# Kernel optimization log

Measured on AMD Instinct MI355X. Metric: run time of the kernel, lower is better.

## Reference

```python
import jax, jax.numpy as jnp
import numpy as np

B, S, D = 4, 2048, 1024


def setup_inputs() -> dict:
    key = jax.random.key(0)
    ks = jax.random.split(key, 9)
    scale = 1.0 / np.sqrt(D)
    v = jax.random.normal(ks[0], (B, S, D), dtype=jnp.float32)
    k = jax.random.normal(ks[1], (B, S, D), dtype=jnp.float32)
    q = jax.random.normal(ks[2], (B, S, D), dtype=jnp.float32)
    # causal boolean mask broadcast over batch: [B, S, S]
    mask = jnp.broadcast_to(jnp.tril(jnp.ones((S, S), dtype=bool)), (B, S, S))
    Wq = jax.random.normal(ks[3], (D, D), dtype=jnp.float32) * scale
    bq = jnp.zeros((D,), dtype=jnp.float32)
    Wk = jax.random.normal(ks[4], (D, D), dtype=jnp.float32) * scale
    bk = jnp.zeros((D,), dtype=jnp.float32)
    Wv = jax.random.normal(ks[5], (D, D), dtype=jnp.float32) * scale
    bv = jnp.zeros((D,), dtype=jnp.float32)
    return {"v": v, "k": k, "q": q, "mask": mask,
            "Wq": Wq, "bq": bq, "Wk": Wk, "bk": bk, "Wv": Wv, "bv": bv}


def reference(v, k, q, mask, Wq, bq, Wk, bk, Wv, bv):
    # Dense projections (flax Dense: x @ W + b)
    qp = jnp.einsum('bsd,de->bse', q, Wq) + bq
    kp = jnp.einsum('bsd,de->bse', k, Wk) + bk
    vp = jnp.einsum('bsd,de->bse', v, Wv) + bv
    inv_sqrt_d = jnp.float32(1.0 / np.sqrt(D))
    scores = jnp.einsum('bqd,bkd->bqk', qp, kp) * inv_sqrt_d  # [B,S,S]
    scores = jnp.where(mask, scores, jnp.float32(-1e10))
    attn = jax.nn.softmax(scores, axis=-1)
    return qp + jnp.einsum('bqk,bkd->bqd', attn, vp)
```

## Files before the change

kernel.cpp:

```cpp
#include <hip/hip_runtime.h>
#include <hip/hip_bf16.h>
#include <stdint.h>
#include <stddef.h>


using bf16 = __hip_bfloat16;
typedef __attribute__((ext_vector_type(8))) short short8;
typedef __attribute__((ext_vector_type(4))) float f32x4;

#define B_ 4
#define S_ 2048
#define D_ 1024
#define NTOK (B_ * S_)
#define NELEM ((size_t)NTOK * D_)

__device__ __forceinline__ float bits_to_f(unsigned short h) {
  union { unsigned int u; float f; } c;
  c.u = ((unsigned int)h) << 16;
  return c.f;
}

__device__ __forceinline__ void gld_lds16(const void* g, void* l) {
  __builtin_amdgcn_global_load_lds(
      (const __attribute__((address_space(1))) unsigned int*)g,
      (__attribute__((address_space(3))) unsigned int*)l, 16, 0, 0);
}

__global__ void detect_kernel(const unsigned short* __restrict__ qraw,
                              int* __restrict__ flag) {
  const int lane = threadIdx.x;
  const float v = fabsf(bits_to_f(qraw[2 * lane]));
  const bool sane = (v < 64.0f) && (v == 0.0f || v > 1e-30f);
  const unsigned long long m = __ballot(sane);
  if (lane == 0) *flag = (__popcll(m) >= 56) ? 1 : 0;
}

__global__ __launch_bounds__(256) void zero_kernel(float* __restrict__ p) {
  p[blockIdx.x * 256 + threadIdx.x] = 0.f;
}

__global__ __launch_bounds__(256) void convert_kernel(
    const void* __restrict__ v, const void* __restrict__ k,
    const void* __restrict__ q, bf16* __restrict__ dst,
    const int* __restrict__ flag) {
  const int z = blockIdx.z;
  const void* src = (z == 0) ? v : (z == 1) ? k : q;
  bf16* d = dst + (size_t)z * NELEM;
  const size_t i = (size_t)blockIdx.x * 256 + threadIdx.x;
  const int mode = *flag;
  if (mode) {
    ((uint4*)d)[i] = ((const uint4*)src)[i];
  } else {
    const float4 a = ((const float4*)src)[2 * i];
    const float4 b = ((const float4*)src)[2 * i + 1];
    __align__(16) bf16 t[8];
    t[0] = __float2bfloat16(a.x); t[1] = __float2bfloat16(a.y);
    t[2] = __float2bfloat16(a.z); t[3] = __float2bfloat16(a.w);
    t[4] = __float2bfloat16(b.x); t[5] = __float2bfloat16(b.y);
    t[6] = __float2bfloat16(b.z); t[7] = __float2bfloat16(b.w);
    ((uint4*)d)[i] = *(const uint4*)t;
  }
}

__global__ __launch_bounds__(256) void transpose_kernel(
    const void* __restrict__ Wq, const void* __restrict__ Wk,
    const void* __restrict__ Wv, bf16* __restrict__ WT,
    const int* __restrict__ flag) {
  __shared__ bf16 t[32][33];
  const int z = blockIdx.z;
  const void* W = (z == 0) ? Wq : (z == 1) ? Wk : Wv;
  bf16* O = WT + (size_t)z * D_ * D_;
  const int bx = blockIdx.x * 32, by = blockIdx.y * 32;
  const int tx = threadIdx.x, ty = threadIdx.y;
  const int mode = *flag;
#pragma unroll
  for (int i = 0; i < 32; i += 8) {
    const size_t idx = (size_t)(by + ty + i) * D_ + bx + tx;
    const float val = mode ? __bfloat162float(((const bf16*)W)[idx])
                           : ((const float*)W)[idx];
    t[ty + i][tx] = __float2bfloat16(val);
  }
  __syncthreads();
#pragma unroll
  for (int i = 0; i < 32; i += 8)
    O[(size_t)(bx + ty + i) * D_ + by + tx] = t[tx][ty + i];
}

__device__ __forceinline__ void gemm128_core(
    const bf16* __restrict__ A, int lda, int m0,
    const bf16* __restrict__ Bt, int ldb, int n0,
    int kEnd, bf16* As, bf16* Bs, f32x4 acc[4][4])
{
  const int tid  = threadIdx.x;
  const int wave = tid >> 6;
  const int lane = tid & 63;
  const int srow = lane >> 2;
  const int scol = (lane & 3) * 8;
  const int wm = (wave & 1) * 64;
  const int wn = (wave >> 1) * 64;
  const int fr = lane & 15;
  const int fk = (lane >> 4) * 8;

  for (int k0 = 0; k0 < kEnd; k0 += 32) {
    __syncthreads();
#pragma unroll
    for (int i = 0; i < 2; ++i) {
      const int r0 = (i * 4 + wave) * 16;
      gld_lds16(A  + (size_t)(m0 + r0 + srow) * lda + k0 + scol, As + r0 * 32);
      gld_lds16(Bt + (size_t)(n0 + r0 + srow) * ldb + k0 + scol, Bs + r0 * 32);
    }
    __syncthreads();
    short8 a[4], b[4];
#pragma unroll
    for (int t = 0; t < 4; ++t) {
      a[t] = *(const short8*)(As + (wm + t * 16 + fr) * 32 + fk);
      b[t] = *(const short8*)(Bs + (wn + t * 16 + fr) * 32 + fk);
    }
#pragma unroll
    for (int mt = 0; mt < 4; ++mt)
#pragma unroll
      for (int nt = 0; nt < 4; ++nt)
        acc[mt][nt] = __builtin_amdgcn_mfma_f32_16x16x32_bf16(
            a[mt], b[nt], acc[mt][nt], 0, 0, 0);
  }
}

__global__ __launch_bounds__(256) void proj_kernel(
    const bf16* __restrict__ xc,
    const bf16* __restrict__ WT,
    const void* __restrict__ bq, const void* __restrict__ bk,
    const void* __restrict__ bv,
    bf16* __restrict__ qp, bf16* __restrict__ kp, bf16* __restrict__ vpt,
    const int* __restrict__ flag)
{
  __shared__ bf16 As[128 * 32];
  __shared__ bf16 Bs[128 * 32];
  const int z = blockIdx.z;
  const bf16* A    = xc + (size_t)(z == 0 ? 2 : (z == 1 ? 1 : 0)) * NELEM;
  const void* bias = (z == 0) ? bq : (z == 1) ? bk : bv;
  const bf16* Bt = WT + (size_t)z * D_ * D_;
  const int m0 = blockIdx.x * 128, n0 = blockIdx.y * 128;
  const int mode = *flag;

  f32x4 acc[4][4] = {};
  gemm128_core(A, D_, m0, Bt, D_, n0, D_, As, Bs, acc);

  const int lane = threadIdx.x & 63, wave = threadIdx.x >> 6;
  const int wm = (wave & 1) * 64, wn = (wave >> 1) * 64;
  const int ccol = lane & 15, crow = (lane >> 4) * 4;
#pragma unroll
  for (int mt = 0; mt < 4; ++mt)
#pragma unroll
    for (int nt = 0; nt < 4; ++nt)
#pragma unroll
      for (int i = 0; i < 4; ++i) {
        const int m = m0 + wm + mt * 16 + crow + i;
        const int n = n0 + wn + nt * 16 + ccol;
        const float bval = mode ? __bfloat162float(((const bf16*)bias)[n])
                                : ((const float*)bias)[n];
        const float val = acc[mt][nt][i] + bval;
        if (z == 0)      qp[(size_t)m * D_ + n] = __float2bfloat16(val);
        else if (z == 1) kp[(size_t)m * D_ + n] = __float2bfloat16(val);
        else {
          const int b = m >> 11, s = m & (S_ - 1);
          vpt[((size_t)b * D_ + n) * S_ + s] = __float2bfloat16(val);
        }
      }
}

__global__ __launch_bounds__(256) void scores_kernel(
    const bf16* __restrict__ qp, const bf16* __restrict__ kp,
    bf16* __restrict__ sc, float* __restrict__ rowsum)
{
  const int m0 = blockIdx.x * 128, n0 = blockIdx.y * 128, bb = blockIdx.z;
  if (n0 > m0) return;
  __shared__ bf16 As[128 * 32];
  __shared__ bf16 Bs[128 * 32];
  const bf16* A  = qp + (size_t)bb * S_ * D_;
  const bf16* Bt = kp + (size_t)bb * S_ * D_;

  f32x4 acc[4][4] = {};
  gemm128_core(A, D_, m0, Bt, D_, n0, D_, As, Bs, acc);

  bf16* out = sc + (size_t)bb * S_ * S_;
  float* rs = rowsum + (size_t)bb * S_;
  const float scale = 0.03125f;
  const float MAXS = 8.0f;
  const int lane = threadIdx.x & 63, wave = threadIdx.x >> 6;
  const int wm = (wave & 1) * 64, wn = (wave >> 1) * 64;
  const int ccol = lane & 15, crow = (lane >> 4) * 4;
#pragma unroll
  for (int mt = 0; mt < 4; ++mt) {
#pragma unroll
    for (int i = 0; i < 4; ++i) {
      const int m = m0 + wm + mt * 16 + crow + i;
      float part = 0.f;
#pragma unroll
      for (int nt = 0; nt < 4; ++nt) {
        const int n = n0 + wn + nt * 16 + ccol;
        float p = 0.f;
        if (n <= m) {
          const bf16 pb = __float2bfloat16(__expf(acc[mt][nt][i] * scale - MAXS));
          p = __bfloat162float(pb);
          out[(size_t)m * S_ + n] = pb;
        } else {
          out[(size_t)m * S_ + n] = __float2bfloat16(0.f);
        }
        part += p;
      }
      part += __shfl_down(part, 8, 64);
      part += __shfl_down(part, 4, 64);
      part += __shfl_down(part, 2, 64);
      part += __shfl_down(part, 1, 64);
      if (ccol == 0) atomicAdd(&rs[m], part);
    }
  }
}

__global__ __launch_bounds__(256) void pv_kernel(
    const bf16* __restrict__ attn, const bf16* __restrict__ vpt,
    const bf16* __restrict__ qp, const float* __restrict__ rowsum,
    void* __restrict__ out, const int* __restrict__ flag)
{
  __shared__ bf16 As[128 * 32];
  __shared__ bf16 Bs[128 * 32];
  const int m0 = (15 - blockIdx.x) * 128;
  const int n0 = blockIdx.y * 128, bb = blockIdx.z;
  const bf16* A  = attn + (size_t)bb * S_ * S_;
  const bf16* Bt = vpt  + (size_t)bb * D_ * S_;
  const int mode = *flag;

  f32x4 acc[4][4] = {};
  gemm128_core(A, S_, m0, Bt, S_, n0, m0 + 128, As, Bs, acc);

  const bf16* qpb = qp + (size_t)bb * S_ * D_;
  const float* rs = rowsum + (size_t)bb * S_;
  const size_t obase = (size_t)bb * S_ * D_;
  const int lane = threadIdx.x & 63, wave = threadIdx.x >> 6;
  const int wm = (wave & 1) * 64, wn = (wave >> 1) * 64;
  const int ccol = lane & 15, crow = (lane >> 4) * 4;
#pragma unroll
  for (int mt = 0; mt < 4; ++mt)
#pragma unroll
    for (int i = 0; i < 4; ++i) {
      const int m = m0 + wm + mt * 16 + crow + i;
      const float inv = 1.f / rs[m];
#pragma unroll
      for (int nt = 0; nt < 4; ++nt) {
        const int n = n0 + wn + nt * 16 + ccol;
        const float val = acc[mt][nt][i] * inv +
                          __bfloat162float(qpb[(size_t)m * D_ + n]);
        const size_t idx = obase + (size_t)m * D_ + n;
        if (mode) ((bf16*)out)[idx] = __float2bfloat16(val);
        else      ((float*)out)[idx] = val;
      }
    }
}

extern "C" void kernel_launch(void* const* d_in, const int* in_sizes, int n_in,
                              void* d_out, int out_size, void* d_ws, size_t ws_size,
                              hipStream_t stream) {
  (void)in_sizes; (void)n_in; (void)out_size; (void)ws_size;
  const void* v  = d_in[0];
  const void* k  = d_in[1];
  const void* q  = d_in[2];
  const void* Wq = d_in[4];
  const void* bq = d_in[5];
  const void* Wk = d_in[6];
  const void* bk = d_in[7];
  const void* Wv = d_in[8];
  const void* bv = d_in[9];

  char* ws = (char*)d_ws;
  int*   flag   = (int*)ws;           ws += 256;
  float* rowsum = (float*)ws;         ws += (size_t)NTOK * 4;
  bf16* WT   = (bf16*)ws;             ws += (size_t)3 * D_ * D_ * 2;
  bf16* qp   = (bf16*)ws;             ws += NELEM * 2;
  bf16* kp   = (bf16*)ws;             ws += NELEM * 2;
  bf16* vpt  = (bf16*)ws;             ws += NELEM * 2;
  bf16* X    = (bf16*)ws;
  bf16* sc   = X;

  detect_kernel<<<dim3(1), dim3(64), 0, stream>>>((const unsigned short*)q, flag);
  zero_kernel<<<dim3(NTOK / 256), dim3(256), 0, stream>>>(rowsum);
  convert_kernel<<<dim3(4096, 1, 3), dim3(256), 0, stream>>>(v, k, q, X, flag);
  transpose_kernel<<<dim3(32, 32, 3), dim3(32, 8), 0, stream>>>(Wq, Wk, Wv, WT, flag);
  proj_kernel<<<dim3(64, 8, 3), dim3(256), 0, stream>>>(
      X, WT, bq, bk, bv, qp, kp, vpt, flag);
  scores_kernel<<<dim3(16, 16, 4), dim3(256), 0, stream>>>(qp, kp, sc, rowsum);
  pv_kernel<<<dim3(16, 8, 4), dim3(256), 0, stream>>>(
      sc, vpt, qp, rowsum, d_out, flag);
}
```

Measured before the change: 406.0 us.

## Double GEMM K-step to 64 with XOR-swizzled LDS and fuse prep kernels

The shared GEMM core now stages 64-wide K slices per iteration instead of 32. The LDS columns are XOR-swizzled so the MFMA fragment reads avoid bank conflicts, and each loop iteration carries twice as many MFMAs per pair of barriers. Separately, the zero, convert and transpose kernels are merged into one prep kernel to cut launch count. LDS per block doubles to 32KB, which could reduce occupancy.

Measured after the change: 390.6 us. 3.8% less time.

```diff
diff --git a/kernel.cpp b/kernel.cpp
--- a/kernel.cpp
+++ b/kernel.cpp
@@ -35,55 +35,58 @@
   if (lane == 0) *flag = (__popcll(m) >= 56) ? 1 : 0;
 }
 
-__global__ __launch_bounds__(256) void zero_kernel(float* __restrict__ p) {
-  p[blockIdx.x * 256 + threadIdx.x] = 0.f;
-}
-
-__global__ __launch_bounds__(256) void convert_kernel(
+__global__ __launch_bounds__(256) void prep_kernel(
     const void* __restrict__ v, const void* __restrict__ k,
-    const void* __restrict__ q, bf16* __restrict__ dst,
-    const int* __restrict__ flag) {
-  const int z = blockIdx.z;
-  const void* src = (z == 0) ? v : (z == 1) ? k : q;
-  bf16* d = dst + (size_t)z * NELEM;
-  const size_t i = (size_t)blockIdx.x * 256 + threadIdx.x;
+    const void* __restrict__ q,
+    const void* __restrict__ Wq, const void* __restrict__ Wk,
+    const void* __restrict__ Wv,
+    bf16* __restrict__ X, bf16* __restrict__ WT,
+    float* __restrict__ rowsum, const int* __restrict__ flag)
+{
+  __shared__ bf16 tbuf[32][33];
+  const int bid = blockIdx.x;
+  const int tid = threadIdx.x;
   const int mode = *flag;
-  if (mode) {
-    ((uint4*)d)[i] = ((const uint4*)src)[i];
+
+  if (bid < 12288) {
+    const int z = bid >> 12;
+    const void* src = (z == 0) ? v : (z == 1) ? k : q;
+    bf16* d = X + (size_t)z * NELEM;
+    const size_t i = (size_t)(bid & 4095) * 256 + tid;
+    if (mode) {
+      ((uint4*)d)[i] = ((const uint4*)src)[i];
+    } else {
+      const float4 a = ((const float4*)src)[2 * i];
+      const float4 b = ((const float4*)src)[2 * i + 1];
+      __align__(16) bf16 t[8];
+      t[0] = __float2bfloat16(a.x); t[1] = __float2bfloat16(a.y);
+      t[2] = __float2bfloat16(a.z); t[3] = __float2bfloat16(a.w);
+      t[4] = __float2bfloat16(b.x); t[5] = __float2bfloat16(b.y);
+      t[6] = __float2bfloat16(b.z); t[7] = __float2bfloat16(b.w);
+      ((uint4*)d)[i] = *(const uint4*)t;
+    }
+  } else if (bid < 15360) {
+    const int t = bid - 12288;
+    const int z = t >> 10;
+    const int tt = t & 1023;
+    const void* W = (z == 0) ? Wq : (z == 1) ? Wk : Wv;
+    bf16* O = WT + (size_t)z * D_ * D_;
+    const int bx = (tt & 31) * 32, by = (tt >> 5) * 32;
+    const int tx = tid & 31, ty = tid >> 5;
+#pragma unroll
+    for (int i = 0; i < 32; i += 8) {
+      const size_t idx = (size_t)(by + ty + i) * D_ + bx + tx;
+      const float val = mode ? __bfloat162float(((const bf16*)W)[idx])
+                             : ((const float*)W)[idx];
+      tbuf[ty + i][tx] = __float2bfloat16(val);
+    }
+    __syncthreads();
+#pragma unroll
+    for (int i = 0; i < 32; i += 8)
+      O[(size_t)(bx + ty + i) * D_ + by + tx] = tbuf[tx][ty + i];
   } else {
-    const float4 a = ((const float4*)src)[2 * i];
-    const float4 b = ((const float4*)src)[2 * i + 1];
-    __align__(16) bf16 t[8];
-    t[0] = __float2bfloat16(a.x); t[1] = __float2bfloat16(a.y);
-    t[2] = __float2bfloat16(a.z); t[3] = __float2bfloat16(a.w);
-    t[4] = __float2bfloat16(b.x); t[5] = __float2bfloat16(b.y);
-    t[6] = __float2bfloat16(b.z); t[7] = __float2bfloat16(b.w);
-    ((uint4*)d)[i] = *(const uint4*)t;
+    rowsum[(bid - 15360) * 256 + tid] = 0.f;
   }
-}
-
-__global__ __launch_bounds__(256) void transpose_kernel(
-    const void* __restrict__ Wq, const void* __restrict__ Wk,
-    const void* __restrict__ Wv, bf16* __restrict__ WT,
-    const int* __restrict__ flag) {
-  __shared__ bf16 t[32][33];
-  const int z = blockIdx.z;
-  const void* W = (z == 0) ? Wq : (z == 1) ? Wk : Wv;
-  bf16* O = WT + (size_t)z * D_ * D_;
-  const int bx = blockIdx.x * 32, by = blockIdx.y * 32;
-  const int tx = threadIdx.x, ty = threadIdx.y;
-  const int mode = *flag;
-#pragma unroll
-  for (int i = 0; i < 32; i += 8) {
-    const size_t idx = (size_t)(by + ty + i) * D_ + bx + tx;
-    const float val = mode ? __bfloat162float(((const bf16*)W)[idx])
-                           : ((const float*)W)[idx];
-    t[ty + i][tx] = __float2bfloat16(val);
-  }
-  __syncthreads();
-#pragma unroll
-  for (int i = 0; i < 32; i += 8)
-    O[(size_t)(bx + ty + i) * D_ + by + tx] = t[tx][ty + i];
 }
 
 __device__ __forceinline__ void gemm128_core(
@@ -94,34 +97,40 @@
   const int tid  = threadIdx.x;
   const int wave = tid >> 6;
   const int lane = tid & 63;
-  const int srow = lane >> 2;
-  const int scol = (lane & 3) * 8;
   const int wm = (wave & 1) * 64;
   const int wn = (wave >> 1) * 64;
   const int fr = lane & 15;
-  const int fk = (lane >> 4) * 8;
-
-  for (int k0 = 0; k0 < kEnd; k0 += 32) {
+  const int q4 = lane >> 4;
+  const int sw = fr & 7;
+  const int srow = lane >> 3;
+  const int scol = ((lane & 7) ^ (lane >> 3)) * 8;
+
+  for (int k0 = 0; k0 < kEnd; k0 += 64) {
     __syncthreads();
 #pragma unroll
-    for (int i = 0; i < 2; ++i) {
-      const int r0 = (i * 4 + wave) * 16;
-      gld_lds16(A  + (size_t)(m0 + r0 + srow) * lda + k0 + scol, As + r0 * 32);
-      gld_lds16(Bt + (size_t)(n0 + r0 + srow) * ldb + k0 + scol, Bs + r0 * 32);
+    for (int i = 0; i < 4; ++i) {
+      const int rb = (i * 4 + wave) * 8;
+      gld_lds16(A  + (size_t)(m0 + rb + srow) * lda + k0 + scol, As + rb * 64);
+      gld_lds16(Bt + (size_t)(n0 + rb + srow) * ldb + k0 + scol, Bs + rb * 64);
     }
     __syncthreads();
-    short8 a[4], b[4];
-#pragma unroll
-    for (int t = 0; t < 4; ++t) {
-      a[t] = *(const short8*)(As + (wm + t * 16 + fr) * 32 + fk);
-      b[t] = *(const short8*)(Bs + (wn + t * 16 + fr) * 32 + fk);
-    }
-#pragma unroll
-    for (int mt = 0; mt < 4; ++mt)
-#pragma unroll
-      for (int nt = 0; nt < 4; ++nt)
-        acc[mt][nt] = __builtin_amdgcn_mfma_f32_16x16x32_bf16(
-            a[mt], b[nt], acc[mt][nt], 0, 0, 0);
+#pragma unroll
+    for (int kk = 0; kk < 64; kk += 32) {
+      const int c0 = (kk >> 3) + q4;
+      const int coff = (c0 ^ sw) * 8;
+      short8 a[4], b[4];
+#pragma unroll
+      for (int t = 0; t < 4; ++t) {
+        a[t] = *(const short8*)(As + (wm + t * 16 + fr) * 64 + coff);
+        b[t] = *(const short8*)(Bs + (wn + t * 16 + fr) * 64 + coff);
+      }
+#pragma unroll
+      for (int mt = 0; mt < 4; ++mt)
+#pragma unroll
+        for (int nt = 0; nt < 4; ++nt)
+          acc[mt][nt] = __builtin_amdgcn_mfma_f32_16x16x32_bf16(
+              a[mt], b[nt], acc[mt][nt], 0, 0, 0);
+    }
   }
 }
 
@@ -133,8 +142,8 @@
     bf16* __restrict__ qp, bf16* __restrict__ kp, bf16* __restrict__ vpt,
     const int* __restrict__ flag)
 {
-  __shared__ bf16 As[128 * 32];
-  __shared__ bf16 Bs[128 * 32];
+  __shared__ bf16 As[128 * 64];
+  __shared__ bf16 Bs[128 * 64];
   const int z = blockIdx.z;
   const bf16* A    = xc + (size_t)(z == 0 ? 2 : (z == 1 ? 1 : 0)) * NELEM;
   const void* bias = (z == 0) ? bq : (z == 1) ? bk : bv;
@@ -174,8 +183,8 @@
 {
   const int m0 = blockIdx.x * 128, n0 = blockIdx.y * 128, bb = blockIdx.z;
   if (n0 > m0) return;
-  __shared__ bf16 As[128 * 32];
-  __shared__ bf16 Bs[128 * 32];
+  __shared__ bf16 As[128 * 64];
+  __shared__ bf16 Bs[128 * 64];
   const bf16* A  = qp + (size_t)bb * S_ * D_;
   const bf16* Bt = kp + (size_t)bb * S_ * D_;
 
@@ -222,8 +231,8 @@
     const bf16* __restrict__ qp, const float* __restrict__ rowsum,
     void* __restrict__ out, const int* __restrict__ flag)
 {
-  __shared__ bf16 As[128 * 32];
-  __shared__ bf16 Bs[128 * 32];
+  __shared__ bf16 As[128 * 64];
+  __shared__ bf16 Bs[128 * 64];
   const int m0 = (15 - blockIdx.x) * 128;
   const int n0 = blockIdx.y * 128, bb = blockIdx.z;
   const bf16* A  = attn + (size_t)bb * S_ * S_;
@@ -282,9 +291,8 @@
   bf16* sc   = X;
 
   detect_kernel<<<dim3(1), dim3(64), 0, stream>>>((const unsigned short*)q, flag);
-  zero_kernel<<<dim3(NTOK / 256), dim3(256), 0, stream>>>(rowsum);
-  convert_kernel<<<dim3(4096, 1, 3), dim3(256), 0, stream>>>(v, k, q, X, flag);
-  transpose_kernel<<<dim3(32, 32, 3), dim3(32, 8), 0, stream>>>(Wq, Wk, Wv, WT, flag);
+  prep_kernel<<<dim3(15392), dim3(256), 0, stream>>>(
+      v, k, q, Wq, Wk, Wv, X, WT, rowsum, flag);
   proj_kernel<<<dim3(64, 8, 3), dim3(256), 0, stream>>>(
       X, WT, bq, bk, bv, qp, kp, vpt, flag);
   scores_kernel<<<dim3(16, 16, 4), dim3(256), 0, stream>>>(qp, kp, sc, rowsum);
```
